# Kernel tuning notes

Hardware: AMD Instinct MI355X
Metric: run time of the kernel (lower is better)

The kernel has to match this reference:

```python
import jax, jax.numpy as jnp
import numpy as np

B, T, H, U, F, K, M = 64, 2048, 1024, 128, 32, 31, 512
PAD = 2 * (K - 1) // 2  # dilation=2, 'same' padding = 30


def setup_inputs() -> dict:
    key = jax.random.key(0)
    ks = jax.random.split(key, 10)
    s = lambda d: 1.0 / np.sqrt(d)
    return {
        "query": jax.random.normal(ks[0], (B, 1, H), dtype=jnp.float32),
        "state": jax.random.uniform(ks[1], (B, T), dtype=jnp.float32),
        "prev_cum": jnp.zeros((B, T), dtype=jnp.float32),
        "memory": jax.random.normal(ks[2], (B, T, M), dtype=jnp.float32),
        "Wq": jax.random.normal(ks[3], (H, U), dtype=jnp.float32) * s(H),
        "bq": jnp.zeros((U,), dtype=jnp.float32),
        "Wm": jax.random.normal(ks[4], (M, U), dtype=jnp.float32) * s(M),
        "bm": jnp.zeros((U,), dtype=jnp.float32),
        "Wl": jax.random.normal(ks[5], (F, U), dtype=jnp.float32) * s(F),
        "bl": jnp.zeros((U,), dtype=jnp.float32),
        "We": jax.random.normal(ks[6], (U, U), dtype=jnp.float32) * s(U),
        "be": jnp.zeros((U,), dtype=jnp.float32),
        "va": jax.random.normal(ks[7], (U,), dtype=jnp.float32),
        "conv_w": jax.random.normal(ks[8], (F, 1, K), dtype=jnp.float32) * s(K),
        "conv_b": jnp.zeros((F,), dtype=jnp.float32),
    }


def reference(query, state, prev_cum, memory, Wq, bq, Wm, bm, Wl, bl, We, be, va, conv_w, conv_b):
    # query projection, keep first time step: [B,1,U]
    pq = (query @ Wq + bq)[:, 0:1, :]
    # processed memory (done in initialize() in torch): [B,T,U]
    pm = memory @ Wm + bm
    # location features: dilated conv over previous alignment, 'same' length
    x = state[:, None, :]  # [B,1,T]
    f = jax.lax.conv_general_dilated(
        x, conv_w, window_strides=(1,), padding=[(PAD, PAD)],
        rhs_dilation=(2,), dimension_numbers=("NCH", "OIH", "NCH"),
    ) + conv_b[None, :, None]                     # [B,F,T]
    pl = jnp.transpose(f, (0, 2, 1)) @ Wl + bl    # [B,T,U]
    # additive energy with extra linear + v_a reduction: [B,T]
    energy = jnp.sum(va * jnp.tanh((pq + pl + pm) @ We + be), axis=2)
    # smoothing (sigmoid) normalization instead of softmax
    sg = jax.nn.sigmoid(energy)
    alignment = sg / jnp.sum(sg, axis=-1, keepdims=True)  # [B,T]
    cum = prev_cum + alignment  # cumulate_weights=True
    # context over PROCESSED memory, matching self.memoery usage: [B,1,U]
    context = cum[:, None, :] @ pm
    return context
```

## Files before the change

### kernel.cpp

```cpp
#include <hip/hip_runtime.h>

#define Bv 64
#define Tv 2048
#define Hv 1024
#define Uv 128
#define Mv 512

typedef __bf16 bf16x8 __attribute__((ext_vector_type(8)));
typedef float f32x4 __attribute__((ext_vector_type(4)));

union U4BF { uint4 u; bf16x8 b; };

#define MFMA(a, b, c) __builtin_amdgcn_mfma_f32_16x16x32_bf16((a), (b), (c), 0, 0, 0)

__device__ __forceinline__ unsigned short f2bf(float f) {
  __bf16 h = (__bf16)f;
  return __builtin_bit_cast(unsigned short, h);
}
__device__ __forceinline__ unsigned int pack2(unsigned short lo, unsigned short hi) {
  return (unsigned int)lo | ((unsigned int)hi << 16);
}

__global__ __launch_bounds__(128) void k1_kernel(const float* __restrict__ query,
                                                 const float* __restrict__ Wq,
                                                 const float* __restrict__ bq,
                                                 const float* __restrict__ Wl,
                                                 const float* __restrict__ bl,
                                                 const float* __restrict__ conv_w,
                                                 const float* __restrict__ conv_b,
                                                 float* __restrict__ pq,
                                                 float* __restrict__ W2,
                                                 float* __restrict__ bias2) {
  const int bx = blockIdx.x;
  const int u = threadIdx.x;
  if (bx < 512) {
    const int b = bx >> 3, c = bx & 7;
    float acc = (c == 0) ? bq[u] : 0.0f;
    const float* q  = query + b * Hv + c * 128;
    const float* wq = Wq + (size_t)c * 128 * Uv;
    #pragma unroll 8
    for (int h = 0; h < 128; ++h) acc = fmaf(q[h], wq[h * Uv + u], acc);
    unsafeAtomicAdd(&pq[b * Uv + u], acc);
  } else {
    float wl[32];
    #pragma unroll
    for (int f = 0; f < 32; ++f) wl[f] = Wl[f * Uv + u];
    for (int k = 0; k < 31; ++k) {
      float acc = 0.0f;
      #pragma unroll
      for (int f = 0; f < 32; ++f) acc = fmaf(conv_w[f * 31 + k], wl[f], acc);
      W2[k * Uv + u] = acc;
    }
    float acc = bl[u];
    #pragma unroll
    for (int f = 0; f < 32; ++f) acc = fmaf(conv_b[f], wl[f], acc);
    bias2[u] = acc;
  }
}

__global__ __launch_bounds__(256) void k2_kernel(const float* __restrict__ pq,
                                                 const float* __restrict__ bias2,
                                                 const float* __restrict__ bm,
                                                 const float* __restrict__ be,
                                                 const float* __restrict__ We,
                                                 const float* __restrict__ W2,
                                                 float* __restrict__ qe,
                                                 float* __restrict__ w3tmp) {
  const int gtid = blockIdx.x * 256 + threadIdx.x;
  const int r = gtid >> 7, n = gtid & 127;
  if (r < 64) {
    float acc = be[n];
    for (int u = 0; u < Uv; ++u)
      acc = fmaf(pq[r * Uv + u] + bias2[u] + bm[u], We[u * Uv + n], acc);
    qe[r * Uv + n] = acc;
  } else {
    const int w = r - 64;
    float acc = 0.0f;
    if (w < 31) {
      for (int u = 0; u < Uv; ++u) acc = fmaf(W2[w * Uv + u], We[u * Uv + n], acc);
    }
    w3tmp[w * Uv + n] = acc;
  }
}

__global__ __launch_bounds__(256) void k3_kernel(const float* __restrict__ Wm,
                                                 const float* __restrict__ We,
                                                 const float* __restrict__ w3tmp,
                                                 unsigned short* __restrict__ WmF,
                                                 unsigned short* __restrict__ WeF,
                                                 unsigned short* __restrict__ W3F) {
  const int gtid = blockIdx.x * 256 + threadIdx.x;
  const int fid = gtid >> 6, lane = gtid & 63;
  const int quad = lane >> 4, l4 = lane & 15;
  float v[8];
  unsigned short* dst;
  if (fid < 128) {
    const int kc = fid >> 3, uj = fid & 7;
    #pragma unroll
    for (int j = 0; j < 8; ++j) v[j] = Wm[(size_t)(kc * 32 + quad * 8 + j) * Uv + uj * 16 + l4];
    dst = WmF + (size_t)fid * 512 + lane * 8;
  } else if (fid < 160) {
    const int f2 = fid - 128;
    const int kc = f2 >> 3, nj = f2 & 7;
    #pragma unroll
    for (int j = 0; j < 8; ++j) v[j] = We[(size_t)(kc * 32 + quad * 8 + j) * Uv + nj * 16 + l4];
    dst = WeF + (size_t)f2 * 512 + lane * 8;
  } else {
    const int nj = fid - 160;
    #pragma unroll
    for (int j = 0; j < 8; ++j) v[j] = w3tmp[(quad * 8 + j) * Uv + nj * 16 + l4];
    dst = W3F + (size_t)nj * 512 + lane * 8;
  }
  uint4 o;
  o.x = pack2(f2bf(v[0]), f2bf(v[1]));
  o.y = pack2(f2bf(v[2]), f2bf(v[3]));
  o.z = pack2(f2bf(v[4]), f2bf(v[5]));
  o.w = pack2(f2bf(v[6]), f2bf(v[7]));
  *(uint4*)dst = o;
}

__global__ __launch_bounds__(256) void main_kernel(
    const float* __restrict__ memory, const unsigned short* __restrict__ WmF,
    const unsigned short* __restrict__ WeF, const unsigned short* __restrict__ W3F,
    const float* __restrict__ qe, const float* __restrict__ state,
    const float* __restrict__ prev_cum, const float* __restrict__ bm,
    const float* __restrict__ va,
    float* __restrict__ P0, float* __restrict__ P1, float* __restrict__ Ssg) {
  const int tid = threadIdx.x;
  const int lane = tid & 63, wid = tid >> 6;
  const int l4 = lane & 15, quad = lane >> 4;
  const int wt = wid >> 1, wu = wid & 1;
  const int b = blockIdx.y, t0 = blockIdx.x * 64;

  __shared__ float sState[124];
  __shared__ float sPc[64];
  __shared__ float sBm[128];
  __shared__ float sVa[128];
  __shared__ float sSg[64];
  __shared__ float blkP0[128], blkP1[128];
  __shared__ float blkSsg;
  __shared__ __align__(16) unsigned short sS[64 * 144];

  for (int i = tid; i < 124; i += 256) {
    int t = t0 - 30 + i;
    sState[i] = (t >= 0 && t < Tv) ? state[b * Tv + t] : 0.0f;
  }
  if (tid < 64) sPc[tid] = prev_cum[b * Tv + t0 + tid];
  for (int i = tid; i < 128; i += 256) {
    sBm[i] = bm[i]; sVa[i] = va[i]; blkP0[i] = 0.0f; blkP1[i] = 0.0f;
  }
  if (tid == 0) blkSsg = 0.0f;

  f32x4 acc[2][4];
  #pragma unroll
  for (int ti = 0; ti < 2; ++ti)
    #pragma unroll
    for (int uj = 0; uj < 4; ++uj) acc[ti][uj] = (f32x4){0.f, 0.f, 0.f, 0.f};

  const float* aBase = memory + ((size_t)b * Tv + t0 + wt * 32 + l4) * Mv + quad * 8;
  const unsigned short* bBase = WmF + (size_t)(wu * 4) * 512 + lane * 8;

  for (int kc = 0; kc < 16; ++kc) {
    float4 a0 = *(const float4*)(aBase + kc * 32);
    float4 a1 = *(const float4*)(aBase + kc * 32 + 4);
    float4 a2 = *(const float4*)(aBase + (size_t)16 * Mv + kc * 32);
    float4 a3 = *(const float4*)(aBase + (size_t)16 * Mv + kc * 32 + 4);
    U4BF bf[4];
    #pragma unroll
    for (int uj = 0; uj < 4; ++uj)
      bf[uj].u = *(const uint4*)(bBase + (size_t)(kc * 8 + uj) * 512);
    bf16x8 af0, af1;
    af0[0] = (__bf16)a0.x; af0[1] = (__bf16)a0.y; af0[2] = (__bf16)a0.z; af0[3] = (__bf16)a0.w;
    af0[4] = (__bf16)a1.x; af0[5] = (__bf16)a1.y; af0[6] = (__bf16)a1.z; af0[7] = (__bf16)a1.w;
    af1[0] = (__bf16)a2.x; af1[1] = (__bf16)a2.y; af1[2] = (__bf16)a2.z; af1[3] = (__bf16)a2.w;
    af1[4] = (__bf16)a3.x; af1[5] = (__bf16)a3.y; af1[6] = (__bf16)a3.z; af1[7] = (__bf16)a3.w;
    #pragma unroll
    for (int uj = 0; uj < 4; ++uj) {
      acc[0][uj] = MFMA(af0, bf[uj].b, acc[0][uj]);
      acc[1][uj] = MFMA(af1, bf[uj].b, acc[1][uj]);
    }
  }

  #pragma unroll
  for (int ti = 0; ti < 2; ++ti) {
    const int rowb = wt * 32 + ti * 16 + quad * 4;
    #pragma unroll
    for (int uj = 0; uj < 4; ++uj) {
      const int col = wu * 64 + uj * 16 + l4;
      #pragma unroll
      for (int r = 0; r < 4; ++r) sS[(rowb + r) * 144 + col] = f2bf(acc[ti][uj][r]);
    }
  }
  __syncthreads();

  const int w = wid;
  f32x4 e[8];
  #pragma unroll
  for (int nj = 0; nj < 8; ++nj) {
    float qv = qe[b * Uv + nj * 16 + l4];
    e[nj] = (f32x4){qv, qv, qv, qv};
  }
  bf16x8 a2f;
  #pragma unroll
  for (int j = 0; j < 8; ++j) {
    int k = quad * 8 + j;
    float v = (k < 31) ? sState[(w * 16 + l4) + 2 * k] : 0.0f;
    a2f[j] = (__bf16)v;
  }
  #pragma unroll
  for (int nj = 0; nj < 8; ++nj) {
    U4BF bb; bb.u = *(const uint4*)(W3F + (size_t)nj * 512 + lane * 8);
    e[nj] = MFMA(a2f, bb.b, e[nj]);
  }
  #pragma unroll
  for (int ks = 0; ks < 4; ++ks) {
    U4BF au;
    au.u = *(const uint4*)&sS[(w * 16 + l4) * 144 + ks * 32 + quad * 8];
    #pragma unroll
    for (int nj = 0; nj < 8; ++nj) {
      U4BF bb; bb.u = *(const uint4*)(WeF + (size_t)(ks * 8 + nj) * 512 + lane * 8);
      e[nj] = MFMA(au.b, bb.b, e[nj]);
    }
  }
  float p[4] = {0.f, 0.f, 0.f, 0.f};
  #pragma unroll
  for (int nj = 0; nj < 8; ++nj) {
    float vav = sVa[nj * 16 + l4];
    #pragma unroll
    for (int r = 0; r < 4; ++r) p[r] = fmaf(vav, tanhf(e[nj][r]), p[r]);
  }
  #pragma unroll
  for (int off = 1; off <= 8; off <<= 1) {
    #pragma unroll
    for (int r = 0; r < 4; ++r) p[r] += __shfl_xor(p[r], off, 64);
  }
  float sgv4[4], sgsum = 0.f;
  #pragma unroll
  for (int r = 0; r < 4; ++r) {
    sgv4[r] = 1.0f / (1.0f + expf(-p[r]));
    sgsum += sgv4[r];
  }
  if (l4 == 0) {
    #pragma unroll
    for (int r = 0; r < 4; ++r) sSg[w * 16 + quad * 4 + r] = sgv4[r];
    atomicAdd(&blkSsg, sgsum);
  }
  __syncthreads();

  float sgl[8], pcl[8];
  #pragma unroll
  for (int ti = 0; ti < 2; ++ti)
    #pragma unroll
    for (int r = 0; r < 4; ++r) {
      int row = wt * 32 + ti * 16 + quad * 4 + r;
      sgl[ti * 4 + r] = sSg[row];
      pcl[ti * 4 + r] = sPc[row];
    }
  #pragma unroll
  for (int uj = 0; uj < 4; ++uj) {
    const int col = wu * 64 + uj * 16 + l4;
    const float bmv = sBm[col];
    float c0 = 0.f, c1 = 0.f;
    #pragma unroll
    for (int ti = 0; ti < 2; ++ti)
      #pragma unroll
      for (int r = 0; r < 4; ++r) {
        float pmv = acc[ti][uj][r] + bmv;
        c0 = fmaf(pcl[ti * 4 + r], pmv, c0);
        c1 = fmaf(sgl[ti * 4 + r], pmv, c1);
      }
    c0 += __shfl_xor(c0, 16, 64); c0 += __shfl_xor(c0, 32, 64);
    c1 += __shfl_xor(c1, 16, 64); c1 += __shfl_xor(c1, 32, 64);
    if (quad == 0) {
      atomicAdd(&blkP0[col], c0);
      atomicAdd(&blkP1[col], c1);
    }
  }
  __syncthreads();
  if (tid < 128) {
    unsafeAtomicAdd(&P0[b * Uv + tid], blkP0[tid]);
    unsafeAtomicAdd(&P1[b * Uv + tid], blkP1[tid]);
  }
  if (tid == 0) unsafeAtomicAdd(&Ssg[b], blkSsg);
}

__global__ __launch_bounds__(128) void finish_kernel(const float* __restrict__ P0,
                                                     const float* __restrict__ P1,
                                                     const float* __restrict__ Ssg,
                                                     float* __restrict__ out) {
  const int b = blockIdx.x, u = threadIdx.x;
  out[b * Uv + u] = P0[b * Uv + u] + P1[b * Uv + u] / Ssg[b];
}

extern "C" void kernel_launch(void* const* d_in, const int* in_sizes, int n_in,
                              void* d_out, int out_size, void* d_ws, size_t ws_size,
                              hipStream_t stream) {
  (void)in_sizes; (void)n_in; (void)out_size; (void)ws_size;
  const float* query    = (const float*)d_in[0];
  const float* state    = (const float*)d_in[1];
  const float* prev_cum = (const float*)d_in[2];
  const float* memory   = (const float*)d_in[3];
  const float* Wq       = (const float*)d_in[4];
  const float* bq       = (const float*)d_in[5];
  const float* Wm       = (const float*)d_in[6];
  const float* bm       = (const float*)d_in[7];
  const float* Wl       = (const float*)d_in[8];
  const float* bl       = (const float*)d_in[9];
  const float* We       = (const float*)d_in[10];
  const float* be       = (const float*)d_in[11];
  const float* va       = (const float*)d_in[12];
  const float* conv_w   = (const float*)d_in[13];
  const float* conv_b   = (const float*)d_in[14];

  float* ws = (float*)d_ws;
  float* P0    = ws;
  float* P1    = ws + 8192;
  float* Ssg   = ws + 16384;
  float* pq    = ws + 16448;
  float* W2    = ws + 24640;
  float* bias2 = ws + 28608;
  float* qe    = ws + 28736;
  float* w3tmp = ws + 36928;
  unsigned short* WmF = (unsigned short*)(ws + 41024);
  unsigned short* WeF = (unsigned short*)(ws + 73792);
  unsigned short* W3F = (unsigned short*)(ws + 81984);

  hipMemsetAsync(d_ws, 0, 24640 * sizeof(float), stream);

  k1_kernel<<<513, 128, 0, stream>>>(query, Wq, bq, Wl, bl, conv_w, conv_b, pq, W2, bias2);
  k2_kernel<<<48, 256, 0, stream>>>(pq, bias2, bm, be, We, W2, qe, w3tmp);
  k3_kernel<<<42, 256, 0, stream>>>(Wm, We, w3tmp, WmF, WeF, W3F);
  main_kernel<<<dim3(Tv / 64, Bv), 256, 0, stream>>>(
      memory, WmF, WeF, W3F, qe, state, prev_cum, bm, va, P0, P1, Ssg);
  finish_kernel<<<Bv, 128, 0, stream>>>(P0, P1, Ssg, (float*)d_out);
}
```

Measured before the change: 465.3 us.

## Double-buffer memory tiles into LDS via async global_load_lds with swizzle

```diff
diff --git a/kernel.cpp b/kernel.cpp
--- a/kernel.cpp
+++ b/kernel.cpp
@@ -12,6 +12,10 @@
 union U4BF { uint4 u; bf16x8 b; };
 
 #define MFMA(a, b, c) __builtin_amdgcn_mfma_f32_16x16x32_bf16((a), (b), (c), 0, 0, 0)
+
+#define GLOAD_LDS16(g, l) __builtin_amdgcn_global_load_lds( \
+    (const __attribute__((address_space(1))) unsigned int*)(g), \
+    (__attribute__((address_space(3))) unsigned int*)(l), 16, 0, 0)
 
 __device__ __forceinline__ unsigned short f2bf(float f) {
   __bf16 h = (__bf16)f;
@@ -140,6 +144,25 @@
   __shared__ float blkP0[128], blkP1[128];
   __shared__ float blkSsg;
   __shared__ __align__(16) unsigned short sS[64 * 144];
+  __shared__ __align__(16) float sA[2][2048];
+
+  const int p0 = tid, p1 = tid + 256;
+  const int sr0 = p0 >> 3, sc0 = (p0 & 7) ^ (sr0 & 7);
+  const int sr1 = p1 >> 3, sc1 = (p1 & 7) ^ (sr1 & 7);
+  const float* g0 = memory + ((size_t)b * Tv + t0 + sr0) * Mv + sc0 * 4;
+  const float* g1 = memory + ((size_t)b * Tv + t0 + sr1) * Mv + sc1 * 4;
+
+  {
+    float* d0 = &sA[0][0] + wid * 256;
+    GLOAD_LDS16(g0, d0);
+    GLOAD_LDS16(g1, d0 + 1024);
+  }
+
+  const unsigned short* bBase = WmF + (size_t)(wu * 4) * 512 + lane * 8;
+  uint4 bc0 = *(const uint4*)(bBase);
+  uint4 bc1 = *(const uint4*)(bBase + 512);
+  uint4 bc2 = *(const uint4*)(bBase + 1024);
+  uint4 bc3 = *(const uint4*)(bBase + 1536);
 
   for (int i = tid; i < 124; i += 256) {
     int t = t0 - 30 + i;
@@ -151,33 +174,57 @@
   }
   if (tid == 0) blkSsg = 0.0f;
 
+  const int r0 = wt * 32 + l4;
+  const int q2 = quad * 2, rx = r0 & 7;
+  const int s00 = r0 * 8 + (q2 ^ rx);
+  const int s01 = r0 * 8 + ((q2 + 1) ^ rx);
+
   f32x4 acc[2][4];
   #pragma unroll
   for (int ti = 0; ti < 2; ++ti)
     #pragma unroll
     for (int uj = 0; uj < 4; ++uj) acc[ti][uj] = (f32x4){0.f, 0.f, 0.f, 0.f};
 
-  const float* aBase = memory + ((size_t)b * Tv + t0 + wt * 32 + l4) * Mv + quad * 8;
-  const unsigned short* bBase = WmF + (size_t)(wu * 4) * 512 + lane * 8;
+  __syncthreads();
 
   for (int kc = 0; kc < 16; ++kc) {
-    float4 a0 = *(const float4*)(aBase + kc * 32);
-    float4 a1 = *(const float4*)(aBase + kc * 32 + 4);
-    float4 a2 = *(const float4*)(aBase + (size_t)16 * Mv + kc * 32);
-    float4 a3 = *(const float4*)(aBase + (size_t)16 * Mv + kc * 32 + 4);
-    U4BF bf[4];
-    #pragma unroll
-    for (int uj = 0; uj < 4; ++uj)
-      bf[uj].u = *(const uint4*)(bBase + (size_t)(kc * 8 + uj) * 512);
+    const int cur = kc & 1;
+    if (kc < 15) {
+      float* d0 = &sA[0][0] + (cur ? 0 : 2048) + wid * 256;
+      GLOAD_LDS16(g0 + (kc + 1) * 32, d0);
+      GLOAD_LDS16(g1 + (kc + 1) * 32, d0 + 1024);
+    }
+    uint4 bn0, bn1, bn2, bn3;
+    if (kc < 15) {
+      const unsigned short* nb = bBase + (size_t)(kc + 1) * 8 * 512;
+      bn0 = *(const uint4*)(nb);
+      bn1 = *(const uint4*)(nb + 512);
+      bn2 = *(const uint4*)(nb + 1024);
+      bn3 = *(const uint4*)(nb + 1536);
+    }
+    const float4* sf = (const float4*)(&sA[0][0]) + (cur ? 512 : 0);
+    float4 a0 = sf[s00];
+    float4 a1 = sf[s01];
+    float4 a2 = sf[s00 + 128];
+    float4 a3 = sf[s01 + 128];
     bf16x8 af0, af1;
     af0[0] = (__bf16)a0.x; af0[1] = (__bf16)a0.y; af0[2] = (__bf16)a0.z; af0[3] = (__bf16)a0.w;
     af0[4] = (__bf16)a1.x; af0[5] = (__bf16)a1.y; af0[6] = (__bf16)a1.z; af0[7] = (__bf16)a1.w;
     af1[0] = (__bf16)a2.x; af1[1] = (__bf16)a2.y; af1[2] = (__bf16)a2.z; af1[3] = (__bf16)a2.w;
     af1[4] = (__bf16)a3.x; af1[5] = (__bf16)a3.y; af1[6] = (__bf16)a3.z; af1[7] = (__bf16)a3.w;
-    #pragma unroll
-    for (int uj = 0; uj < 4; ++uj) {
-      acc[0][uj] = MFMA(af0, bf[uj].b, acc[0][uj]);
-      acc[1][uj] = MFMA(af1, bf[uj].b, acc[1][uj]);
+    U4BF bb0, bb1, bb2, bb3;
+    bb0.u = bc0; bb1.u = bc1; bb2.u = bc2; bb3.u = bc3;
+    acc[0][0] = MFMA(af0, bb0.b, acc[0][0]);
+    acc[1][0] = MFMA(af1, bb0.b, acc[1][0]);
+    acc[0][1] = MFMA(af0, bb1.b, acc[0][1]);
+    acc[1][1] = MFMA(af1, bb1.b, acc[1][1]);
+    acc[0][2] = MFMA(af0, bb2.b, acc[0][2]);
+    acc[1][2] = MFMA(af1, bb2.b, acc[1][2]);
+    acc[0][3] = MFMA(af0, bb3.b, acc[0][3]);
+    acc[1][3] = MFMA(af1, bb3.b, acc[1][3]);
+    if (kc < 15) {
+      bc0 = bn0; bc1 = bn1; bc2 = bn2; bc3 = bn3;
+      __syncthreads();
     }
   }
 
```

After: 454.8 us. 1.02x faster.

## Stage memory tiles through LDS with async global_load_lds double buffering

Applied to the files above, without the earlier changes.

```diff
diff --git a/kernel.cpp b/kernel.cpp
--- a/kernel.cpp
+++ b/kernel.cpp
@@ -12,6 +12,10 @@
 union U4BF { uint4 u; bf16x8 b; };
 
 #define MFMA(a, b, c) __builtin_amdgcn_mfma_f32_16x16x32_bf16((a), (b), (c), 0, 0, 0)
+
+#define GLOAD_LDS16(g, l) __builtin_amdgcn_global_load_lds( \
+    (const __attribute__((address_space(1))) unsigned int*)(g), \
+    (__attribute__((address_space(3))) unsigned int*)(l), 16, 0, 0)
 
 __device__ __forceinline__ unsigned short f2bf(float f) {
   __bf16 h = (__bf16)f;
@@ -139,7 +143,21 @@
   __shared__ float sSg[64];
   __shared__ float blkP0[128], blkP1[128];
   __shared__ float blkSsg;
-  __shared__ __align__(16) unsigned short sS[64 * 144];
+  __shared__ __align__(16) char smem[32768];
+  float* sAf = (float*)smem;
+  unsigned short* sS = (unsigned short*)smem;
+
+  const int p0 = tid, p1 = tid + 256;
+  const int sr0 = p0 >> 3, sc0 = (p0 & 7) ^ (sr0 & 7);
+  const int sr1 = p1 >> 3, sc1 = (p1 & 7) ^ (sr1 & 7);
+  const float* g0 = memory + ((size_t)b * Tv + t0 + sr0) * Mv + sc0 * 4;
+  const float* g1 = memory + ((size_t)b * Tv + t0 + sr1) * Mv + sc1 * 4;
+
+  {
+    float* d = sAf + wid * 256;
+    GLOAD_LDS16(g0, d);           GLOAD_LDS16(g1, d + 1024);
+    GLOAD_LDS16(g0 + 32, d + 2048); GLOAD_LDS16(g1 + 32, d + 3072);
+  }
 
   for (int i = tid; i < 124; i += 256) {
     int t = t0 - 30 + i;
@@ -151,34 +169,64 @@
   }
   if (tid == 0) blkSsg = 0.0f;
 
+  const int r0 = wt * 32 + l4;
+  const int q2 = quad * 2, rx = r0 & 7;
+  const int s00 = r0 * 8 + (q2 ^ rx);
+  const int s01 = r0 * 8 + ((q2 + 1) ^ rx);
+
   f32x4 acc[2][4];
   #pragma unroll
   for (int ti = 0; ti < 2; ++ti)
     #pragma unroll
     for (int uj = 0; uj < 4; ++uj) acc[ti][uj] = (f32x4){0.f, 0.f, 0.f, 0.f};
 
-  const float* aBase = memory + ((size_t)b * Tv + t0 + wt * 32 + l4) * Mv + quad * 8;
   const unsigned short* bBase = WmF + (size_t)(wu * 4) * 512 + lane * 8;
 
-  for (int kc = 0; kc < 16; ++kc) {
-    float4 a0 = *(const float4*)(aBase + kc * 32);
-    float4 a1 = *(const float4*)(aBase + kc * 32 + 4);
-    float4 a2 = *(const float4*)(aBase + (size_t)16 * Mv + kc * 32);
-    float4 a3 = *(const float4*)(aBase + (size_t)16 * Mv + kc * 32 + 4);
-    U4BF bf[4];
-    #pragma unroll
-    for (int uj = 0; uj < 4; ++uj)
-      bf[uj].u = *(const uint4*)(bBase + (size_t)(kc * 8 + uj) * 512);
+  auto chunk = [&](const uint4& B0, const uint4& B1, const uint4& B2, const uint4& B3,
+                   int base) {
+    const float4* sf = (const float4*)(sAf + base);
+    float4 a0 = sf[s00];
+    float4 a1 = sf[s01];
+    float4 a2 = sf[s00 + 128];
+    float4 a3 = sf[s01 + 128];
     bf16x8 af0, af1;
     af0[0] = (__bf16)a0.x; af0[1] = (__bf16)a0.y; af0[2] = (__bf16)a0.z; af0[3] = (__bf16)a0.w;
     af0[4] = (__bf16)a1.x; af0[5] = (__bf16)a1.y; af0[6] = (__bf16)a1.z; af0[7] = (__bf16)a1.w;
     af1[0] = (__bf16)a2.x; af1[1] = (__bf16)a2.y; af1[2] = (__bf16)a2.z; af1[3] = (__bf16)a2.w;
     af1[4] = (__bf16)a3.x; af1[5] = (__bf16)a3.y; af1[6] = (__bf16)a3.z; af1[7] = (__bf16)a3.w;
-    #pragma unroll
-    for (int uj = 0; uj < 4; ++uj) {
-      acc[0][uj] = MFMA(af0, bf[uj].b, acc[0][uj]);
-      acc[1][uj] = MFMA(af1, bf[uj].b, acc[1][uj]);
-    }
+    U4BF u0, u1, u2, u3;
+    u0.u = B0; u1.u = B1; u2.u = B2; u3.u = B3;
+    acc[0][0] = MFMA(af0, u0.b, acc[0][0]);
+    acc[1][0] = MFMA(af1, u0.b, acc[1][0]);
+    acc[0][1] = MFMA(af0, u1.b, acc[0][1]);
+    acc[1][1] = MFMA(af1, u1.b, acc[1][1]);
+    acc[0][2] = MFMA(af0, u2.b, acc[0][2]);
+    acc[1][2] = MFMA(af1, u2.b, acc[1][2]);
+    acc[0][3] = MFMA(af0, u3.b, acc[0][3]);
+    acc[1][3] = MFMA(af1, u3.b, acc[1][3]);
+  };
+
+  __syncthreads();
+
+  for (int oc = 0; oc < 8; ++oc) {
+    const int rb = (oc & 1) * 4096;
+    if (oc < 7) {
+      const int wb = ((oc + 1) & 1) * 4096;
+      float* d = sAf + wb + wid * 256;
+      const float* ga = g0 + (oc + 1) * 64;
+      const float* gb = g1 + (oc + 1) * 64;
+      GLOAD_LDS16(ga, d);           GLOAD_LDS16(gb, d + 1024);
+      GLOAD_LDS16(ga + 32, d + 2048); GLOAD_LDS16(gb + 32, d + 3072);
+    }
+    const unsigned short* pB0 = bBase + (size_t)(2 * oc) * 4096;
+    const unsigned short* pB1 = pB0 + 4096;
+    uint4 b00 = *(const uint4*)pB0;          uint4 b01 = *(const uint4*)(pB0 + 512);
+    uint4 b02 = *(const uint4*)(pB0 + 1024); uint4 b03 = *(const uint4*)(pB0 + 1536);
+    uint4 b10 = *(const uint4*)pB1;          uint4 b11 = *(const uint4*)(pB1 + 512);
+    uint4 b12 = *(const uint4*)(pB1 + 1024); uint4 b13 = *(const uint4*)(pB1 + 1536);
+    chunk(b00, b01, b02, b03, rb);
+    chunk(b10, b11, b12, b13, rb + 2048);
+    __syncthreads();
   }
 
   #pragma unroll
```

Measured after the change: 457.9 us. About the same (-1.6%).

## Retile memory GEMM per-wave 16 rows, prefetch A ring, use fast tanh/sigmoid

Applied to the files above, without the earlier changes.

```diff
diff --git a/kernel.cpp b/kernel.cpp
--- a/kernel.cpp
+++ b/kernel.cpp
@@ -19,6 +19,13 @@
 }
 __device__ __forceinline__ unsigned int pack2(unsigned short lo, unsigned short hi) {
   return (unsigned int)lo | ((unsigned int)hi << 16);
+}
+__device__ __forceinline__ float tanh_fast(float x) {
+  float e = __expf(2.0f * x);
+  return 1.0f - 2.0f / (e + 1.0f);
+}
+__device__ __forceinline__ float sigmoid_fast(float x) {
+  return 1.0f / (1.0f + __expf(-x));
 }
 
 __global__ __launch_bounds__(128) void k1_kernel(const float* __restrict__ query,
@@ -129,7 +136,6 @@
   const int tid = threadIdx.x;
   const int lane = tid & 63, wid = tid >> 6;
   const int l4 = lane & 15, quad = lane >> 4;
-  const int wt = wid >> 1, wu = wid & 1;
   const int b = blockIdx.y, t0 = blockIdx.x * 64;
 
   __shared__ float sState[124];
@@ -151,44 +157,62 @@
   }
   if (tid == 0) blkSsg = 0.0f;
 
-  f32x4 acc[2][4];
-  #pragma unroll
-  for (int ti = 0; ti < 2; ++ti)
-    #pragma unroll
-    for (int uj = 0; uj < 4; ++uj) acc[ti][uj] = (f32x4){0.f, 0.f, 0.f, 0.f};
-
-  const float* aBase = memory + ((size_t)b * Tv + t0 + wt * 32 + l4) * Mv + quad * 8;
-  const unsigned short* bBase = WmF + (size_t)(wu * 4) * 512 + lane * 8;
-
-  for (int kc = 0; kc < 16; ++kc) {
-    float4 a0 = *(const float4*)(aBase + kc * 32);
-    float4 a1 = *(const float4*)(aBase + kc * 32 + 4);
-    float4 a2 = *(const float4*)(aBase + (size_t)16 * Mv + kc * 32);
-    float4 a3 = *(const float4*)(aBase + (size_t)16 * Mv + kc * 32 + 4);
-    U4BF bf[4];
-    #pragma unroll
-    for (int uj = 0; uj < 4; ++uj)
-      bf[uj].u = *(const uint4*)(bBase + (size_t)(kc * 8 + uj) * 512);
-    bf16x8 af0, af1;
-    af0[0] = (__bf16)a0.x; af0[1] = (__bf16)a0.y; af0[2] = (__bf16)a0.z; af0[3] = (__bf16)a0.w;
-    af0[4] = (__bf16)a1.x; af0[5] = (__bf16)a1.y; af0[6] = (__bf16)a1.z; af0[7] = (__bf16)a1.w;
-    af1[0] = (__bf16)a2.x; af1[1] = (__bf16)a2.y; af1[2] = (__bf16)a2.z; af1[3] = (__bf16)a2.w;
-    af1[4] = (__bf16)a3.x; af1[5] = (__bf16)a3.y; af1[6] = (__bf16)a3.z; af1[7] = (__bf16)a3.w;
-    #pragma unroll
-    for (int uj = 0; uj < 4; ++uj) {
-      acc[0][uj] = MFMA(af0, bf[uj].b, acc[0][uj]);
-      acc[1][uj] = MFMA(af1, bf[uj].b, acc[1][uj]);
-    }
-  }
-
-  #pragma unroll
-  for (int ti = 0; ti < 2; ++ti) {
-    const int rowb = wt * 32 + ti * 16 + quad * 4;
-    #pragma unroll
-    for (int uj = 0; uj < 4; ++uj) {
-      const int col = wu * 64 + uj * 16 + l4;
+  f32x4 acc[8];
+  #pragma unroll
+  for (int uj = 0; uj < 8; ++uj) acc[uj] = (f32x4){0.f, 0.f, 0.f, 0.f};
+
+  const float* aBase = memory + ((size_t)b * Tv + t0 + wid * 16 + l4) * Mv + quad * 8;
+  const unsigned short* bBase = WmF + lane * 8;
+
+  float4 A0[4], A1[4];
+  #pragma unroll
+  for (int s = 0; s < 4; ++s) {
+    const float* p = aBase + s * 32;
+    A0[s] = *(const float4*)(p);
+    A1[s] = *(const float4*)(p + 4);
+  }
+
+  #define PH1_STEP(kc, slot, REFILL)                                          \
+    {                                                                         \
+      float4 a0 = A0[slot], a1 = A1[slot];                                    \
+      if (REFILL) {                                                           \
+        const float* p = aBase + ((kc) + 4) * 32;                             \
+        A0[slot] = *(const float4*)(p);                                       \
+        A1[slot] = *(const float4*)(p + 4);                                   \
+      }                                                                       \
+      bf16x8 af;                                                              \
+      af[0] = (__bf16)a0.x; af[1] = (__bf16)a0.y;                             \
+      af[2] = (__bf16)a0.z; af[3] = (__bf16)a0.w;                             \
+      af[4] = (__bf16)a1.x; af[5] = (__bf16)a1.y;                             \
+      af[6] = (__bf16)a1.z; af[7] = (__bf16)a1.w;                             \
+      const unsigned short* pb = bBase + (size_t)(kc) * 4096;                 \
+      _Pragma("unroll")                                                       \
+      for (int uj = 0; uj < 8; ++uj) {                                        \
+        U4BF bb; bb.u = *(const uint4*)(pb + uj * 512);                       \
+        acc[uj] = MFMA(af, bb.b, acc[uj]);                                    \
+      }                                                                       \
+    }
+
+  for (int h = 0; h < 3; ++h) {
+    const int k0 = 4 * h;
+    PH1_STEP(k0 + 0, 0, true)
+    PH1_STEP(k0 + 1, 1, true)
+    PH1_STEP(k0 + 2, 2, true)
+    PH1_STEP(k0 + 3, 3, true)
+  }
+  PH1_STEP(12, 0, false)
+  PH1_STEP(13, 1, false)
+  PH1_STEP(14, 2, false)
+  PH1_STEP(15, 3, false)
+  #undef PH1_STEP
+
+  {
+    const int rowb = wid * 16 + quad * 4;
+    #pragma unroll
+    for (int uj = 0; uj < 8; ++uj) {
+      const int col = uj * 16 + l4;
       #pragma unroll
-      for (int r = 0; r < 4; ++r) sS[(rowb + r) * 144 + col] = f2bf(acc[ti][uj][r]);
+      for (int r = 0; r < 4; ++r) sS[(rowb + r) * 144 + col] = f2bf(acc[uj][r]);
     }
   }
   __syncthreads();
@@ -227,7 +251,7 @@
   for (int nj = 0; nj < 8; ++nj) {
     float vav = sVa[nj * 16 + l4];
     #pragma unroll
-    for (int r = 0; r < 4; ++r) p[r] = fmaf(vav, tanhf(e[nj][r]), p[r]);
+    for (int r = 0; r < 4; ++r) p[r] = fmaf(vav, tanh_fast(e[nj][r]), p[r]);
   }
   #pragma unroll
   for (int off = 1; off <= 8; off <<= 1) {
@@ -237,7 +261,7 @@
   float sgv4[4], sgsum = 0.f;
   #pragma unroll
   for (int r = 0; r < 4; ++r) {
-    sgv4[r] = 1.0f / (1.0f + expf(-p[r]));
+    sgv4[r] = sigmoid_fast(p[r]);
     sgsum += sgv4[r];
   }
   if (l4 == 0) {
@@ -247,28 +271,24 @@
   }
   __syncthreads();
 
-  float sgl[8], pcl[8];
-  #pragma unroll
-  for (int ti = 0; ti < 2; ++ti)
-    #pragma unroll
-    for (int r = 0; r < 4; ++r) {
-      int row = wt * 32 + ti * 16 + quad * 4 + r;
-      sgl[ti * 4 + r] = sSg[row];
-      pcl[ti * 4 + r] = sPc[row];
-    }
-  #pragma unroll
-  for (int uj = 0; uj < 4; ++uj) {
-    const int col = wu * 64 + uj * 16 + l4;
+  float sgl[4], pcl[4];
+  #pragma unroll
+  for (int r = 0; r < 4; ++r) {
+    int row = wid * 16 + quad * 4 + r;
+    sgl[r] = sSg[row];
+    pcl[r] = sPc[row];
+  }
+  #pragma unroll
+  for (int uj = 0; uj < 8; ++uj) {
+    const int col = uj * 16 + l4;
     const float bmv = sBm[col];
     float c0 = 0.f, c1 = 0.f;
     #pragma unroll
-    for (int ti = 0; ti < 2; ++ti)
-      #pragma unroll
-      for (int r = 0; r < 4; ++r) {
-        float pmv = acc[ti][uj][r] + bmv;
-        c0 = fmaf(pcl[ti * 4 + r], pmv, c0);
-        c1 = fmaf(sgl[ti * 4 + r], pmv, c1);
-      }
+    for (int r = 0; r < 4; ++r) {
+      float pmv = acc[uj][r] + bmv;
+      c0 = fmaf(pcl[r], pmv, c0);
+      c1 = fmaf(sgl[r], pmv, c1);
+    }
     c0 += __shfl_xor(c0, 16, 64); c0 += __shfl_xor(c0, 32, 64);
     c1 += __shfl_xor(c1, 16, 64); c1 += __shfl_xor(c1, 32, 64);
     if (quad == 0) {
```

Result: slower. 497.7 us (+7.0%).
